# Kernel tuning notes

Measured on AMD Instinct MI355X. Metric: run time of the kernel, lower is better.

## Reference

```python
import jax, jax.numpy as jnp
import numpy as np

B, LU, LV, D = 16, 2048, 2048, 1024


def setup_inputs() -> dict:
    key = jax.random.key(0)
    ku, kv, kl, kw = jax.random.split(key, 4)
    u = jax.random.normal(ku, (B, LU, D), dtype=jnp.float32)
    v = jax.random.normal(kv, (B, LV, D), dtype=jnp.float32)
    # padding mask: True = masked position; every batch keeps >= LV//2 valid tokens
    lengths = jax.random.randint(kl, (B,), LV // 2, LV + 1)
    v_mask = jnp.arange(LV)[None, :] >= lengths[:, None]  # [B, LV] bool
    # Linear(input_size=D, output_size=D) parameters
    W = jax.random.normal(kw, (D, D), dtype=jnp.float32) * (1.0 / np.sqrt(D))
    b = jnp.zeros((D,), dtype=jnp.float32)
    return {"u": u, "v": v, "v_mask": v_mask, "W": W, "b": b}


def reference(u, v, v_mask, W, b):
    # shared ReLU-projected bilinear attention
    u_ = jax.nn.relu(u @ W.T + b)            # [B, Lu, D]
    v_ = jax.nn.relu(v @ W.T + b)            # [B, Lv, D]
    alpha = jnp.einsum("bud,bvd->buv", u_, v_)  # [B, Lu, Lv]
    alpha = jnp.where(v_mask[:, None, :], -jnp.inf, alpha)
    alpha = jax.nn.softmax(alpha, axis=-1)
    return jnp.einsum("buv,bvd->bud", alpha, v)  # [B, Lu, D]
```

## Files before the change

### kernel.cpp

```cpp
#include <hip/hip_runtime.h>
#include <math.h>

#define B_  16
#define LU_ 2048
#define LV_ 2048
#define D_  1024
#define NT_ (LV_ / 128)
#define MB_ (1024ull * 1024ull)

typedef __attribute__((ext_vector_type(8))) short ush8;
typedef __attribute__((ext_vector_type(8))) _Float16 f16x8;
typedef __attribute__((ext_vector_type(4))) float f32x4;

__device__ __forceinline__ unsigned short f2h(float x) {
    _Float16 h = (_Float16)x;
    return __builtin_bit_cast(unsigned short, h);
}

__device__ __forceinline__ void gload_lds16(const void* g, void* l) {
    __builtin_amdgcn_global_load_lds(
        (const __attribute__((address_space(1))) void*)g,
        (__attribute__((address_space(3))) void*)l, 16, 0, 0);
}

__global__ void lengths_kernel(const void* __restrict__ mask, int* __restrict__ lengths) {
    __shared__ int viol;
    __shared__ int cnt[B_];
    const int t = threadIdx.x;
    if (t == 0) viol = 0;
    if (t < B_) cnt[t] = 0;
    __syncthreads();
    const unsigned char* mb = (const unsigned char*)mask;
    int local = 0;
    for (int i = t; i < B_ * LV_ - 1; i += 256) {
        if (((i + 1) % LV_) != 0) {
            if (mb[i] != 0 && mb[i + 1] == 0) local++;
        }
    }
    if (local) atomicAdd(&viol, local);
    __syncthreads();
    const bool is_i32 = (viol > 0);
    const int b = t >> 4, s = t & 15;
    int c = 0;
    if (is_i32) {
        const int* mi = (const int*)mask;
        for (int v2 = s; v2 < LV_; v2 += 16) c += (mi[b * LV_ + v2] == 0) ? 1 : 0;
    } else {
        for (int v2 = s; v2 < LV_; v2 += 16) c += (mb[b * LV_ + v2] == 0) ? 1 : 0;
    }
    atomicAdd(&cnt[b], c);
    __syncthreads();
    if (t < B_) lengths[t] = cnt[t];
}

__global__ __launch_bounds__(256) void cvt_kernel(
    const float* __restrict__ X, unsigned short* __restrict__ Y, long n8) {
    const long stride = (long)gridDim.x * 256;
    for (long i = (long)blockIdx.x * 256 + threadIdx.x; i < n8; i += stride) {
        float4 x0 = ((const float4*)X)[i * 2];
        float4 x1 = ((const float4*)X)[i * 2 + 1];
        float xv[8] = {x0.x, x0.y, x0.z, x0.w, x1.x, x1.y, x1.z, x1.w};
        ush8 h;
#pragma unroll
        for (int j = 0; j < 8; j++) h[j] = (short)f2h(xv[j]);
        ((ush8*)Y)[i] = h;
    }
}

__global__ __launch_bounds__(256, 2) void proj_kernel(
    const unsigned short* __restrict__ Xf, const unsigned short* __restrict__ Wf,
    const float* __restrict__ bias, const int* __restrict__ lengths, int is_v,
    unsigned short* __restrict__ Yf) {
    if (is_v) {
        const int bb = blockIdx.x >> 4;
        const int lv0 = (blockIdx.x & 15) * 128;
        if (lv0 >= lengths[bb]) return;
    }
    __shared__ alignas(16) unsigned short sA[128 * 32], sB[128 * 32];
    const int t = threadIdx.x, lane = t & 63, w = t >> 6;
    const int fr = lane & 15, fg = lane >> 4;
    const int row0 = blockIdx.x * 128, col0 = blockIdx.y * 128;

    const int sr0 = w * 16 + (lane >> 2);
    const int sr1 = 64 + sr0;
    const int c0 = (lane & 3) ^ ((sr0 >> 1) & 3);
    const int c1 = (lane & 3) ^ ((sr1 >> 1) & 3);
    const size_t ao0 = (size_t)(row0 + sr0) * D_ + c0 * 8;
    const size_t ao1 = (size_t)(row0 + sr1) * D_ + c1 * 8;
    const size_t bo0 = (size_t)(col0 + sr0) * D_ + c0 * 8;
    const size_t bo1 = (size_t)(col0 + sr1) * D_ + c1 * 8;
    const int db0 = (w * 16) * 32;
    const int db1 = (64 + w * 16) * 32;

    int aoff[2], boff[8];
#pragma unroll
    for (int m = 0; m < 2; m++) {
        const int r = w * 32 + m * 16 + fr;
        aoff[m] = r * 32 + (fg ^ ((r >> 1) & 3)) * 8;
    }
#pragma unroll
    for (int n = 0; n < 8; n++) {
        const int r = n * 16 + fr;
        boff[n] = r * 32 + (fg ^ ((r >> 1) & 3)) * 8;
    }

    const f32x4 fzero = {0.f, 0.f, 0.f, 0.f};
    f32x4 acc[2][8];
#pragma unroll
    for (int m = 0; m < 2; m++)
#pragma unroll
        for (int n = 0; n < 8; n++) acc[m][n] = fzero;

    for (int k0 = 0; k0 < D_; k0 += 32) {
        __syncthreads();
        gload_lds16(Xf + ao0 + k0, &sA[db0]);
        gload_lds16(Xf + ao1 + k0, &sA[db1]);
        gload_lds16(Wf + bo0 + k0, &sB[db0]);
        gload_lds16(Wf + bo1 + k0, &sB[db1]);
        __syncthreads();
        const f16x8 a0 = *(const f16x8*)&sA[aoff[0]];
        const f16x8 a1 = *(const f16x8*)&sA[aoff[1]];
#pragma unroll
        for (int n = 0; n < 8; n++) {
            const f16x8 bv = *(const f16x8*)&sB[boff[n]];
            acc[0][n] = __builtin_amdgcn_mfma_f32_16x16x32_f16(a0, bv, acc[0][n], 0, 0, 0);
            acc[1][n] = __builtin_amdgcn_mfma_f32_16x16x32_f16(a1, bv, acc[1][n], 0, 0, 0);
        }
    }

#pragma unroll
    for (int m = 0; m < 2; m++)
#pragma unroll
        for (int n = 0; n < 8; n++) {
            const int col = col0 + n * 16 + fr;
            const float bv = bias[col];
#pragma unroll
            for (int j = 0; j < 4; j++) {
                const int row = row0 + w * 32 + m * 16 + fg * 4 + j;
                const float y = fmaxf(acc[m][n][j] + bv, 0.f);
                Yf[(size_t)row * D_ + col] = f2h(y);
            }
        }
}

__global__ __launch_bounds__(256) void transpose_v_kernel(
    const float* __restrict__ V, unsigned short* __restrict__ VT,
    unsigned short* __restrict__ Vraw) {
    __shared__ unsigned short s[64 * 72];
    const int b = blockIdx.z;
    const int v0 = blockIdx.x * 64, d0 = blockIdx.y * 64;
    const int t = threadIdx.x;
    {
        const int r = t >> 2, q = (t & 3) * 16;
        const float* src = V + ((size_t)b * LV_ + v0 + r) * D_ + d0 + q;
        unsigned short hb[16];
#pragma unroll
        for (int i = 0; i < 4; i++) {
            float4 x = ((const float4*)src)[i];
            hb[i * 4 + 0] = f2h(x.x);
            hb[i * 4 + 1] = f2h(x.y);
            hb[i * 4 + 2] = f2h(x.z);
            hb[i * 4 + 3] = f2h(x.w);
        }
#pragma unroll
        for (int j = 0; j < 16; j++) s[r * 72 + q + j] = hb[j];
        unsigned short* rdst = Vraw + ((size_t)b * LV_ + v0 + r) * D_ + d0 + q;
        ((ush8*)rdst)[0] = *(ush8*)&hb[0];
        ((ush8*)rdst)[1] = *(ush8*)&hb[8];
    }
    __syncthreads();
    {
        const int d = t >> 2, vq = (t & 3) * 16;
        ush8 t0, t1;
#pragma unroll
        for (int j = 0; j < 8; j++) t0[j] = (short)s[(vq + j) * 72 + d];
#pragma unroll
        for (int j = 0; j < 8; j++) t1[j] = (short)s[(vq + 8 + j) * 72 + d];
        unsigned short* dst = VT + ((size_t)b * D_ + d0 + d) * LV_ + v0 + vq;
        ((ush8*)dst)[0] = t0;
        ((ush8*)dst)[1] = t1;
    }
}

__global__ __launch_bounds__(256, 2) void attn_logits_kernel(
    const unsigned short* __restrict__ Uf, const unsigned short* __restrict__ Vf,
    const int* __restrict__ lengths,
    unsigned short* __restrict__ Pp, float* __restrict__ m_used,
    float* __restrict__ Z_used) {
    __shared__ alignas(16) unsigned short sU[128 * 32], sV[128 * 32];
    const int b = blockIdx.z, ut = blockIdx.x, vt = blockIdx.y;
    const int t = threadIdx.x, lane = t & 63, w = t >> 6;
    const int fr = lane & 15, fg = lane >> 4;
    const int length = lengths[b];
    const int row0 = ut * 128, col0 = vt * 128;

    if (col0 >= length) {
        if (t < 128) {
            const size_t row = (size_t)b * LU_ + row0 + t;
            m_used[row * NT_ + vt] = -__builtin_inff();
            Z_used[row * NT_ + vt] = 0.f;
        }
        return;
    }

    const int sr0 = w * 16 + (lane >> 2);
    const int sr1 = 64 + sr0;
    const int c0 = (lane & 3) ^ ((sr0 >> 1) & 3);
    const int c1 = (lane & 3) ^ ((sr1 >> 1) & 3);
    const size_t uo0 = ((size_t)b * LU_ + row0 + sr0) * D_ + c0 * 8;
    const size_t uo1 = ((size_t)b * LU_ + row0 + sr1) * D_ + c1 * 8;
    const size_t vo0 = ((size_t)b * LV_ + col0 + sr0) * D_ + c0 * 8;
    const size_t vo1 = ((size_t)b * LV_ + col0 + sr1) * D_ + c1 * 8;
    const int db0 = (w * 16) * 32;
    const int db1 = (64 + w * 16) * 32;

    int aoff[2], boff[8];
#pragma unroll
    for (int m = 0; m < 2; m++) {
        const int r = w * 32 + m * 16 + fr;
        aoff[m] = r * 32 + (fg ^ ((r >> 1) & 3)) * 8;
    }
#pragma unroll
    for (int n = 0; n < 8; n++) {
        const int r = n * 16 + fr;
        boff[n] = r * 32 + (fg ^ ((r >> 1) & 3)) * 8;
    }

    const f32x4 fzero = {0.f, 0.f, 0.f, 0.f};
    f32x4 acc[2][8];
#pragma unroll
    for (int m = 0; m < 2; m++)
#pragma unroll
        for (int n = 0; n < 8; n++) acc[m][n] = fzero;

    for (int k0 = 0; k0 < D_; k0 += 32) {
        __syncthreads();
        gload_lds16(Uf + uo0 + k0, &sU[db0]);
        gload_lds16(Uf + uo1 + k0, &sU[db1]);
        gload_lds16(Vf + vo0 + k0, &sV[db0]);
        gload_lds16(Vf + vo1 + k0, &sV[db1]);
        __syncthreads();
        const f16x8 a0 = *(const f16x8*)&sU[aoff[0]];
        const f16x8 a1 = *(const f16x8*)&sU[aoff[1]];
#pragma unroll
        for (int n = 0; n < 8; n++) {
            const f16x8 bv = *(const f16x8*)&sV[boff[n]];
            acc[0][n] = __builtin_amdgcn_mfma_f32_16x16x32_f16(a0, bv, acc[0][n], 0, 0, 0);
            acc[1][n] = __builtin_amdgcn_mfma_f32_16x16x32_f16(a1, bv, acc[1][n], 0, 0, 0);
        }
    }

#pragma unroll
    for (int m = 0; m < 2; m++) {
        float mt[4] = {-__builtin_inff(), -__builtin_inff(), -__builtin_inff(), -__builtin_inff()};
#pragma unroll
        for (int n = 0; n < 8; n++) {
            const int col = col0 + n * 16 + fr;
            if (col < length) {
#pragma unroll
                for (int j = 0; j < 4; j++) mt[j] = fmaxf(mt[j], acc[m][n][j]);
            }
        }
#pragma unroll
        for (int d = 1; d < 16; d <<= 1) {
#pragma unroll
            for (int j = 0; j < 4; j++) mt[j] = fmaxf(mt[j], __shfl_xor(mt[j], d));
        }
        float rs[4] = {0.f, 0.f, 0.f, 0.f};
#pragma unroll
        for (int n = 0; n < 8; n++) {
            const int col = col0 + n * 16 + fr;
            const bool valid = (col < length);
#pragma unroll
            for (int j = 0; j < 4; j++) {
                const float p = valid ? __expf(acc[m][n][j] - mt[j]) : 0.f;
                rs[j] += p;
                const size_t row = (size_t)b * LU_ + row0 + w * 32 + m * 16 + fg * 4 + j;
                Pp[row * LV_ + col] = f2h(p);
            }
        }
#pragma unroll
        for (int d = 1; d < 16; d <<= 1) {
#pragma unroll
            for (int j = 0; j < 4; j++) rs[j] += __shfl_xor(rs[j], d);
        }
        if (fr == 0) {
#pragma unroll
            for (int j = 0; j < 4; j++) {
                const size_t row = (size_t)b * LU_ + row0 + w * 32 + m * 16 + fg * 4 + j;
                m_used[row * NT_ + vt] = mt[j];
                Z_used[row * NT_ + vt] = rs[j];
            }
        }
    }
}

__global__ __launch_bounds__(256) void stats_combine_kernel(
    const float* __restrict__ m_used, const float* __restrict__ Z_used,
    float* __restrict__ Sc) {
    const int row = blockIdx.x * 256 + threadIdx.x;
    float mv[NT_];
    float m = -__builtin_inff();
#pragma unroll
    for (int i = 0; i < NT_; i++) {
        mv[i] = m_used[(size_t)row * NT_ + i];
        m = fmaxf(m, mv[i]);
    }
    float ev[NT_];
    float z = 0.f;
#pragma unroll
    for (int i = 0; i < NT_; i++) {
        ev[i] = __expf(mv[i] - m);
        z += Z_used[(size_t)row * NT_ + i] * ev[i];
    }
    const float inv = 1.f / z;
#pragma unroll
    for (int i = 0; i < NT_; i++) Sc[(size_t)row * NT_ + i] = ev[i] * inv;
}

__global__ __launch_bounds__(256, 2) void pv_gemm_kernel(
    const unsigned short* __restrict__ Pp, const unsigned short* __restrict__ VT,
    const float* __restrict__ Sc, const int* __restrict__ lengths,
    float* __restrict__ Out) {
    __shared__ alignas(16) unsigned short sA[128 * 64], sB[128 * 64];
    const int b = blockIdx.z, bm = blockIdx.x, bn = blockIdx.y;
    const int t = threadIdx.x, lane = t & 63, w = t >> 6;
    const int wr = (w >> 1) * 64, wc = (w & 1) * 64;
    const int fr = lane & 15, fg = lane >> 4;
    const int length = lengths[b];
    const int ntv = (length + 127) >> 7;

    size_t aog[4], bog[4];
    int dbs[4];
#pragma unroll
    for (int i = 0; i < 4; i++) {
        const int r = w * 32 + i * 8 + (lane >> 3);
        const int cg = (lane & 7) ^ (r & 7);
        aog[i] = ((size_t)b * LU_ + bm * 128 + r) * LV_ + cg * 8;
        bog[i] = ((size_t)b * D_ + bn * 128 + r) * LV_ + cg * 8;
        dbs[i] = (w * 32 + i * 8) * 64;
    }
    int aoff[2][4], boff[2][4];
#pragma unroll
    for (int kk = 0; kk < 2; kk++) {
#pragma unroll
        for (int m = 0; m < 4; m++) {
            const int r = wr + m * 16 + fr;
            aoff[kk][m] = r * 64 + (((kk * 4 + fg) ^ (r & 7))) * 8;
        }
#pragma unroll
        for (int n = 0; n < 4; n++) {
            const int r = wc + n * 16 + fr;
            boff[kk][n] = r * 64 + (((kk * 4 + fg) ^ (r & 7))) * 8;
        }
    }

    const f32x4 fzero = {0.f, 0.f, 0.f, 0.f};
    f32x4 acc[4][4];
#pragma unroll
    for (int m = 0; m < 4; m++)
#pragma unroll
        for (int n = 0; n < 4; n++) acc[m][n] = fzero;

    const int rowb = bm * 128 + wr + fg * 4;

#pragma unroll 1
    for (int vt = 0; vt < ntv; ++vt) {
        f32x4 part[4][4];
#pragma unroll
        for (int m = 0; m < 4; m++)
#pragma unroll
            for (int n = 0; n < 4; n++) part[m][n] = fzero;

#pragma unroll 1
        for (int kb = 0; kb < 2; ++kb) {
            const int k0 = vt * 128 + kb * 64;
            __syncthreads();
#pragma unroll
            for (int i = 0; i < 4; i++) {
                gload_lds16(Pp + aog[i] + k0, &sA[dbs[i]]);
                gload_lds16(VT + bog[i] + k0, &sB[dbs[i]]);
            }
            __syncthreads();
#pragma unroll
            for (int kk = 0; kk < 2; kk++) {
                f16x8 af[4];
#pragma unroll
                for (int m = 0; m < 4; m++) af[m] = *(const f16x8*)&sA[aoff[kk][m]];
#pragma unroll
                for (int n = 0; n < 4; n++) {
                    const f16x8 bv = *(const f16x8*)&sB[boff[kk][n]];
#pragma unroll
                    for (int m = 0; m < 4; m++)
                        part[m][n] = __builtin_amdgcn_mfma_f32_16x16x32_f16(af[m], bv, part[m][n], 0, 0, 0);
                }
            }
        }
        float sc[4][4];
#pragma unroll
        for (int m = 0; m < 4; m++)
#pragma unroll
            for (int j = 0; j < 4; j++)
                sc[m][j] = Sc[((size_t)b * LU_ + rowb + m * 16 + j) * NT_ + vt];
#pragma unroll
        for (int m = 0; m < 4; m++)
#pragma unroll
            for (int n = 0; n < 4; n++)
#pragma unroll
                for (int j = 0; j < 4; j++)
                    acc[m][n][j] += sc[m][j] * part[m][n][j];
    }

    float* Ob = Out + (size_t)b * LU_ * D_;
#pragma unroll
    for (int m = 0; m < 4; m++) {
        const int rbase = bm * 128 + wr + m * 16 + fg * 4;
#pragma unroll
        for (int n = 0; n < 4; n++) {
            const int col = bn * 128 + wc + n * 16 + fr;
#pragma unroll
            for (int j = 0; j < 4; j++)
                Ob[(size_t)(rbase + j) * D_ + col] = acc[m][n][j];
        }
    }
}

extern "C" void kernel_launch(void* const* d_in, const int* in_sizes, int n_in,
                              void* d_out, int out_size, void* d_ws, size_t ws_size,
                              hipStream_t stream) {
    (void)in_sizes; (void)n_in; (void)out_size; (void)ws_size;
    const float* u    = (const float*)d_in[0];
    const float* v    = (const float*)d_in[1];
    const void*  vm   = d_in[2];
    const float* W    = (const float*)d_in[3];
    const float* bias = (const float*)d_in[4];
    float* out = (float*)d_out;
    char* ws = (char*)d_ws;

    unsigned short* Pp    = (unsigned short*)(ws + 0 * MB_);
    unsigned short* vT    = (unsigned short*)(ws + 128 * MB_);
    unsigned short* u_f   = (unsigned short*)(ws + 192 * MB_);
    unsigned short* v_f   = (unsigned short*)(ws + 256 * MB_);
    unsigned short* vraw  = (unsigned short*)(ws + 320 * MB_);
    unsigned short* xs_u  = (unsigned short*)(ws + 384 * MB_);
    unsigned short* W_f   = (unsigned short*)(ws + 448 * MB_);
    int*   lengths = (int*)(ws + 450 * MB_);
    float* m_used  = (float*)(ws + 451 * MB_);
    float* Z_used  = (float*)(ws + 453 * MB_);
    float* Sc      = (float*)(ws + 455 * MB_);

    const long nW8 = (long)D_ * D_ / 8;
    const long nX8 = (long)B_ * LU_ * D_ / 8;

    lengths_kernel<<<1, 256, 0, stream>>>(vm, lengths);
    cvt_kernel<<<512, 256, 0, stream>>>(W, W_f, nW8);
    cvt_kernel<<<4096, 256, 0, stream>>>(u, xs_u, nX8);
    proj_kernel<<<dim3(B_ * LU_ / 128, D_ / 128), 256, 0, stream>>>(
        xs_u, W_f, bias, lengths, 0, u_f);
    transpose_v_kernel<<<dim3(LV_ / 64, D_ / 64, B_), 256, 0, stream>>>(v, vT, vraw);
    proj_kernel<<<dim3(B_ * LV_ / 128, D_ / 128), 256, 0, stream>>>(
        vraw, W_f, bias, lengths, 1, v_f);
    attn_logits_kernel<<<dim3(LU_ / 128, NT_, B_), 256, 0, stream>>>(
        u_f, v_f, lengths, Pp, m_used, Z_used);
    stats_combine_kernel<<<B_ * LU_ / 256, 256, 0, stream>>>(m_used, Z_used, Sc);
    pv_gemm_kernel<<<dim3(LU_ / 128, D_ / 128, B_), 256, 0, stream>>>(Pp, vT, Sc, lengths, out);
}
```

Before: 666.1 us.

## Fold softmax tile scale into P fragments and drop partial accumulators

```diff
diff --git a/kernel.cpp b/kernel.cpp
--- a/kernel.cpp
+++ b/kernel.cpp
@@ -318,11 +318,12 @@
     for (int i = 0; i < NT_; i++) Sc[(size_t)row * NT_ + i] = ev[i] * inv;
 }
 
-__global__ __launch_bounds__(256, 2) void pv_gemm_kernel(
+__global__ __launch_bounds__(256, 4) void pv_gemm_kernel(
     const unsigned short* __restrict__ Pp, const unsigned short* __restrict__ VT,
     const float* __restrict__ Sc, const int* __restrict__ lengths,
     float* __restrict__ Out) {
     __shared__ alignas(16) unsigned short sA[128 * 64], sB[128 * 64];
+    __shared__ float sSc[128 * NT_];
     const int b = blockIdx.z, bm = blockIdx.x, bn = blockIdx.y;
     const int t = threadIdx.x, lane = t & 63, w = t >> 6;
     const int wr = (w >> 1) * 64, wc = (w & 1) * 64;
@@ -330,6 +331,14 @@
     const int length = lengths[b];
     const int ntv = (length + 127) >> 7;
 
+    {
+        const float* scg = Sc + ((size_t)b * LU_ + bm * 128) * NT_;
+#pragma unroll
+        for (int i = 0; i < (128 * NT_) / 256; i++)
+            sSc[i * 256 + t] = scg[i * 256 + t];
+    }
+    __syncthreads();
+
     size_t aog[4], bog[4];
     int dbs[4];
 #pragma unroll
@@ -362,15 +371,15 @@
 #pragma unroll
         for (int n = 0; n < 4; n++) acc[m][n] = fzero;
 
-    const int rowb = bm * 128 + wr + fg * 4;
-
 #pragma unroll 1
     for (int vt = 0; vt < ntv; ++vt) {
-        f32x4 part[4][4];
-#pragma unroll
-        for (int m = 0; m < 4; m++)
-#pragma unroll
-            for (int n = 0; n < 4; n++) part[m][n] = fzero;
+        f16x8 scv[4];
+#pragma unroll
+        for (int m = 0; m < 4; m++) {
+            const _Float16 sh = (_Float16)sSc[(wr + m * 16 + fr) * NT_ + vt];
+#pragma unroll
+            for (int j = 0; j < 8; j++) scv[m][j] = sh;
+        }
 
 #pragma unroll 1
         for (int kb = 0; kb < 2; ++kb) {
@@ -386,29 +395,17 @@
             for (int kk = 0; kk < 2; kk++) {
                 f16x8 af[4];
 #pragma unroll
-                for (int m = 0; m < 4; m++) af[m] = *(const f16x8*)&sA[aoff[kk][m]];
+                for (int m = 0; m < 4; m++)
+                    af[m] = (*(const f16x8*)&sA[aoff[kk][m]]) * scv[m];
 #pragma unroll
                 for (int n = 0; n < 4; n++) {
                     const f16x8 bv = *(const f16x8*)&sB[boff[kk][n]];
 #pragma unroll
                     for (int m = 0; m < 4; m++)
-                        part[m][n] = __builtin_amdgcn_mfma_f32_16x16x32_f16(af[m], bv, part[m][n], 0, 0, 0);
+                        acc[m][n] = __builtin_amdgcn_mfma_f32_16x16x32_f16(af[m], bv, acc[m][n], 0, 0, 0);
                 }
             }
         }
-        float sc[4][4];
-#pragma unroll
-        for (int m = 0; m < 4; m++)
-#pragma unroll
-            for (int j = 0; j < 4; j++)
-                sc[m][j] = Sc[((size_t)b * LU_ + rowb + m * 16 + j) * NT_ + vt];
-#pragma unroll
-        for (int m = 0; m < 4; m++)
-#pragma unroll
-            for (int n = 0; n < 4; n++)
-#pragma unroll
-                for (int j = 0; j < 4; j++)
-                    acc[m][n][j] += sc[m][j] * part[m][n][j];
     }
 
     float* Ob = Out + (size_t)b * LU_ * D_;
```

After: 613.2 us. -7.9%, faster.
